# Kernel tuning notes

Hardware: AMD Instinct MI355X
Metric: run time of the kernel (lower is better)

## Reference

```python
import jax, jax.numpy as jnp
import numpy as np

D_MODEL = 768
D_COND = 128
N_LAYERS = 6
D_STATE = 16
D_CONV = 4
EXPAND = 2
D_INNER = EXPAND * D_MODEL            # 1536
DT_RANK = (D_MODEL + 15) // 16        # 48
BATCH, SEQ = 2, 1024
EPS = 1e-5


def setup_inputs() -> dict:
    key = jax.random.key(0)
    ks = iter(jax.random.split(key, 24))
    rn = lambda shape, s=0.02: jax.random.normal(next(ks), shape, dtype=jnp.float32) * s
    inp = {}
    inp["x"] = jax.random.normal(next(ks), (BATCH, SEQ, D_MODEL), dtype=jnp.float32)
    inp["condition"] = jax.random.normal(next(ks), (BATCH, D_COND), dtype=jnp.float32)
    # per-layer Mamba params, stacked on leading layer dim
    inp["in_proj_w"] = rn((N_LAYERS, 2 * D_INNER, D_MODEL))
    inp["conv_w"] = rn((N_LAYERS, D_INNER, D_CONV), 0.1)
    inp["conv_b"] = jnp.zeros((N_LAYERS, D_INNER), jnp.float32)
    inp["x_proj_w"] = rn((N_LAYERS, DT_RANK + 2 * D_STATE, D_INNER))
    inp["dt_proj_w"] = rn((N_LAYERS, D_INNER, DT_RANK), 0.1)
    inp["dt_proj_b"] = jnp.full((N_LAYERS, D_INNER), -4.0, jnp.float32)  # softplus -> small dt
    inp["A_log"] = jnp.tile(jnp.log(jnp.arange(1, D_STATE + 1, dtype=jnp.float32))[None, None, :], (N_LAYERS, D_INNER, 1))
    inp["D_skip"] = jnp.ones((N_LAYERS, D_INNER), jnp.float32)
    inp["out_proj_w"] = rn((N_LAYERS, D_MODEL, D_INNER))
    # post-residual LayerNorm affine per layer
    inp["norm_w"] = jnp.ones((N_LAYERS, D_MODEL), jnp.float32)
    inp["norm_b"] = jnp.zeros((N_LAYERS, D_MODEL), jnp.float32)
    # AdaLN: condition -> (scale, shift)
    inp["adaln_w"] = rn((N_LAYERS, 2 * D_MODEL, D_COND))
    inp["adaln_b"] = jnp.zeros((N_LAYERS, 2 * D_MODEL), jnp.float32)
    inp["final_norm_w"] = jnp.ones((D_MODEL,), jnp.float32)
    inp["final_norm_b"] = jnp.zeros((D_MODEL,), jnp.float32)
    return inp


def _ln(h, w, b):
    mu = jnp.mean(h, -1, keepdims=True)
    var = jnp.mean(jnp.square(h - mu), -1, keepdims=True)
    return (h - mu) * jax.lax.rsqrt(var + EPS) * w + b


def _ln_noaffine(h):
    mu = jnp.mean(h, -1, keepdims=True)
    var = jnp.mean(jnp.square(h - mu), -1, keepdims=True)
    return (h - mu) * jax.lax.rsqrt(var + EPS)


def _mamba(x, in_w, cw, cb, xp_w, dtp_w, dtp_b, A_log, D_skip, out_w):
    b, l, _ = x.shape
    xz = jnp.einsum('bld,ed->ble', x, in_w)                 # [b,l,2*di]
    xc, z = jnp.split(xz, 2, axis=-1)
    # causal depthwise conv over time
    xc_t = jnp.transpose(xc, (0, 2, 1))                     # [b,di,l]
    xc_t = jax.lax.conv_general_dilated(
        xc_t, cw[:, None, :], window_strides=(1,), padding=[(D_CONV - 1, 0)],
        dimension_numbers=('NCH', 'OIH', 'NCH'), feature_group_count=D_INNER)
    xc = jnp.transpose(xc_t + cb[None, :, None], (0, 2, 1))  # [b,l,di]
    xc = jax.nn.silu(xc)
    dbc = jnp.einsum('bld,ed->ble', xc, xp_w)                # [b,l,dt_rank+2*ds]
    dt = dbc[..., :DT_RANK]
    Bm = dbc[..., DT_RANK:DT_RANK + D_STATE]                 # [b,l,ds]
    Cm = dbc[..., DT_RANK + D_STATE:]                        # [b,l,ds]
    dt = jax.nn.softplus(jnp.einsum('blr,dr->bld', dt, dtp_w) + dtp_b)  # [b,l,di]
    A = -jnp.exp(A_log)                                      # [di,ds]

    def step(h, ts):
        dt_t, B_t, C_t, x_t = ts                             # [b,di],[b,ds],[b,ds],[b,di]
        dA = jnp.exp(dt_t[:, :, None] * A)                   # [b,di,ds]
        h = dA * h + (dt_t * x_t)[:, :, None] * B_t[:, None, :]
        y = jnp.sum(h * C_t[:, None, :], axis=-1)            # [b,di]
        return h, y

    h0 = jnp.zeros((b, D_INNER, D_STATE), x.dtype)
    ts = (jnp.transpose(dt, (1, 0, 2)), jnp.transpose(Bm, (1, 0, 2)),
          jnp.transpose(Cm, (1, 0, 2)), jnp.transpose(xc, (1, 0, 2)))
    h_final, y = jax.lax.scan(step, h0, ts)
    y = jnp.transpose(y, (1, 0, 2)) + D_skip * xc            # [b,l,di]
    y = y * jax.nn.silu(z)
    out = jnp.einsum('bld,ed->ble', y, out_w)                # [b,l,dm]
    return out, h_final


def reference(x, condition, in_proj_w, conv_w, conv_b, x_proj_w, dt_proj_w, dt_proj_b,
              A_log, D_skip, out_proj_w, norm_w, norm_b, adaln_w, adaln_b,
              final_norm_w, final_norm_b):
    h = x
    states = []
    for i in range(N_LAYERS):
        residual = h
        m, st = _mamba(h, in_proj_w[i], conv_w[i], conv_b[i], x_proj_w[i],
                       dt_proj_w[i], dt_proj_b[i], A_log[i], D_skip[i], out_proj_w[i])
        h = _ln(residual + m, norm_w[i], norm_b[i])
        ss = condition @ adaln_w[i].T + adaln_b[i]            # [b,2*dm]
        scale, shift = jnp.split(ss, 2, axis=-1)
        h = _ln_noaffine(h) * (1.0 + scale[:, None, :]) + shift[:, None, :]
        states.append(st)
    h = _ln(h, final_norm_w, final_norm_b)
    return h, jnp.stack(states)
```

## Files before the change

### kernel.cpp

```cpp
#include <hip/hip_runtime.h>
#include <hip/hip_bf16.h>

#define NL 6
#define DM 768
#define DI 1536
#define DS 16
#define NRANK 48
#define DBC 80
#define BATCH 2
#define SEQ 1024
#define NTOK (BATCH*SEQ)
#define NCHUNK 64
#define CHLEN 16
#define XKS 8
#define XKC (DI/XKS)

typedef __attribute__((ext_vector_type(8))) short short8;
typedef __attribute__((ext_vector_type(8))) unsigned short ushort8v;
typedef __attribute__((ext_vector_type(4))) float f32x4;
typedef __attribute__((ext_vector_type(4))) unsigned short ushort4v;

__device__ inline unsigned short f2bf(float f) {
  union { float f; unsigned u; } x; x.f = f;
  unsigned r = x.u + 0x7FFF + ((x.u >> 16) & 1);
  return (unsigned short)(r >> 16);
}
__device__ inline float bf2f(unsigned short s) {
  union { unsigned u; float f; } x; x.u = ((unsigned)s) << 16;
  return x.f;
}

__device__ inline void gl_lds16(const unsigned short* g, unsigned short* l) {
  __builtin_amdgcn_global_load_lds(
      (const __attribute__((address_space(1))) unsigned int*)(g),
      (__attribute__((address_space(3))) unsigned int*)(l),
      16, 0, 0);
}

#define V_X   (NTOK * DM / 8)
#define V_INW (NL * 2 * DI * DM / 8)
#define V_OUW (NL * DM * DI / 8)
#define V_XPW (NL * DBC * DI / 8)
#define V_DTW (NL * DI * 64 / 8)
#define V_NA  (NL * DI * DS / 8)
#define V_DTA (NTOK * 64 / 8)
#define V_ALL (V_X + V_INW + V_OUW + V_XPW + V_DTW + V_NA + V_DTA)

__device__ inline ushort8v cvt8v(f32x4 a, f32x4 b) {
  union { ushort8v u8; __hip_bfloat162 h[4]; } u;
  float2 p;
  p.x = a[0]; p.y = a[1]; u.h[0] = __float22bfloat162_rn(p);
  p.x = a[2]; p.y = a[3]; u.h[1] = __float22bfloat162_rn(p);
  p.x = b[0]; p.y = b[1]; u.h[2] = __float22bfloat162_rn(p);
  p.x = b[2]; p.y = b[3]; u.h[3] = __float22bfloat162_rn(p);
  return u.u8;
}
__device__ inline void cvt8_store(const float* s, unsigned short* d, int i) {
  f32x4 a = ((const f32x4*)s)[i * 2];
  f32x4 b = ((const f32x4*)s)[i * 2 + 1];
  ((ushort8v*)d)[i] = cvt8v(a, b);
}

__global__ __launch_bounds__(256) void cvt_k(
    const float* __restrict__ x, const float* __restrict__ inw,
    const float* __restrict__ ouw, const float* __restrict__ xpw,
    const float* __restrict__ dtpw, const float* __restrict__ alog,
    unsigned short* __restrict__ xb, unsigned short* __restrict__ inwb,
    unsigned short* __restrict__ ouwb, unsigned short* __restrict__ xpwb,
    unsigned short* __restrict__ dtwb, float* __restrict__ na,
    unsigned short* __restrict__ dtA) {
  for (int i = blockIdx.x * 256 + threadIdx.x; i < V_ALL; i += gridDim.x * 256) {
    int k = i;
    if (k < V_X) { cvt8_store(x, xb, k); continue; }
    k -= V_X;
    if (k < V_INW) { cvt8_store(inw, inwb, k); continue; }
    k -= V_INW;
    if (k < V_OUW) { cvt8_store(ouw, ouwb, k); continue; }
    k -= V_OUW;
    if (k < V_XPW) { cvt8_store(xpw, xpwb, k); continue; }
    k -= V_XPW;
    if (k < V_DTW) {
      int col8 = (k & 7) * 8;
      int row = k >> 3;
      ushort8v u8;
      if (col8 < NRANK) {
        const float* src = dtpw + (size_t)row * NRANK + col8;
        f32x4 a = *(const f32x4*)src;
        f32x4 b = *(const f32x4*)(src + 4);
        u8 = cvt8v(a, b);
      } else {
        u8 = (ushort8v){0,0,0,0,0,0,0,0};
      }
      *(ushort8v*)&dtwb[(size_t)row * 64 + col8] = u8;
      continue;
    }
    k -= V_DTW;
    if (k < V_NA) {
      f32x4 a = ((const f32x4*)alog)[k * 2];
      f32x4 b = ((const f32x4*)alog)[k * 2 + 1];
      f32x4 ra, rb;
#pragma unroll
      for (int e = 0; e < 4; e++) { ra[e] = -__expf(a[e]); rb[e] = -__expf(b[e]); }
      ((f32x4*)na)[k * 2] = ra;
      ((f32x4*)na)[k * 2 + 1] = rb;
      continue;
    }
    k -= V_NA;
    ((ushort8v*)dtA)[k] = (ushort8v){0,0,0,0,0,0,0,0};
  }
}

__global__ __launch_bounds__(256) void ada_k(const float* __restrict__ cond,
                                             const float* __restrict__ aw,
                                             const float* __restrict__ ab,
                                             float* __restrict__ ss) {
  int idx = blockIdx.x * 256 + threadIdx.x;
  int e = idx % (2 * DM);
  int b = (idx / (2 * DM)) % BATCH;
  int l = idx / (BATCH * 2 * DM);
  const float* c = cond + b * 128;
  const float* wp = aw + ((size_t)l * (2 * DM) + e) * 128;
  float s = ab[l * (2 * DM) + e];
  for (int k = 0; k < 128; k++) s = fmaf(c[k], wp[k], s);
  ss[idx] = s;
}

__global__ __launch_bounds__(256) void bt128b_k(
    const unsigned short* __restrict__ A, int lda,
    const unsigned short* __restrict__ W, int ldw,
    unsigned short* __restrict__ C, int ldc,
    int K) {
  __shared__ __align__(16) unsigned short As[3][128 * 32];
  __shared__ __align__(16) unsigned short Ws[3][128 * 32];
  const int tid = threadIdx.x;
  const int bm = blockIdx.y * 128;
  const int bn = blockIdx.x * 128;
  const int lane = tid & 63;
  const int wv = tid >> 6;
  const int wm = (wv >> 1) * 64;
  const int wn = (wv & 1) * 64;
  const int fr = lane & 15;
  const int fs = lane >> 4;

  const int r0 = tid >> 2;
  const int s0 = (tid & 3) ^ (r0 & 3);

  const unsigned short* gA0 = A + (size_t)(bm + r0) * lda + s0 * 8;
  const unsigned short* gA1 = A + (size_t)(bm + r0 + 64) * lda + s0 * 8;
  const unsigned short* gW0 = W + (size_t)(bn + r0) * ldw + s0 * 8;
  const unsigned short* gW1 = W + (size_t)(bn + r0 + 64) * ldw + s0 * 8;

  f32x4 acc[4][4];
#pragma unroll
  for (int i = 0; i < 4; i++)
#pragma unroll
    for (int j = 0; j < 4; j++) acc[i][j] = (f32x4){0.f, 0.f, 0.f, 0.f};

  const int nk = K >> 5;
  gl_lds16(gA0, &As[0][0] + tid * 8);
  gl_lds16(gA1, &As[0][2048] + tid * 8);
  gl_lds16(gW0, &Ws[0][0] + tid * 8);
  gl_lds16(gW1, &Ws[0][2048] + tid * 8);
  if (nk > 1) {
    gl_lds16(gA0 + 32, &As[1][0] + tid * 8);
    gl_lds16(gA1 + 32, &As[1][2048] + tid * 8);
    gl_lds16(gW0 + 32, &Ws[1][0] + tid * 8);
    gl_lds16(gW1 + 32, &Ws[1][2048] + tid * 8);
  }

  for (int kk = 0; kk < nk; kk++) {
    const int b = kk % 3;
    if (kk + 2 < nk) {
      const int k0 = (kk + 2) * 32;
      const int nb = (kk + 2) % 3;
      gl_lds16(gA0 + k0, &As[nb][0] + tid * 8);
      gl_lds16(gA1 + k0, &As[nb][2048] + tid * 8);
      gl_lds16(gW0 + k0, &Ws[nb][0] + tid * 8);
      gl_lds16(gW1 + k0, &Ws[nb][2048] + tid * 8);
    }
    const int ahead = (nk - 1 - kk >= 2) ? 2 : (nk - 1 - kk);
    if (ahead == 2)      asm volatile("s_waitcnt vmcnt(8)" : : : "memory");
    else if (ahead == 1) asm volatile("s_waitcnt vmcnt(4)" : : : "memory");
    else                 asm volatile("s_waitcnt vmcnt(0)" : : : "memory");
    __builtin_amdgcn_s_barrier();
    __builtin_amdgcn_sched_barrier(0);

    short8 af[4], bf[4];
#pragma unroll
    for (int i = 0; i < 4; i++) {
      int rowa = wm + i * 16 + fr;
      af[i] = *(const short8*)&As[b][rowa * 32 + ((fs ^ (rowa & 3)) * 8)];
      int rowb = wn + i * 16 + fr;
      bf[i] = *(const short8*)&Ws[b][rowb * 32 + ((fs ^ (rowb & 3)) * 8)];
    }
#pragma unroll
    for (int i = 0; i < 4; i++)
#pragma unroll
      for (int j = 0; j < 4; j++)
        acc[i][j] = __builtin_amdgcn_mfma_f32_16x16x32_bf16(af[i], bf[j], acc[i][j], 0, 0, 0);

    __builtin_amdgcn_s_barrier();
  }

#pragma unroll
  for (int i = 0; i < 4; i++) {
#pragma unroll
    for (int j = 0; j < 4; j++) {
#pragma unroll
      for (int r = 0; r < 4; r++) {
        int row = bm + wm + i * 16 + fs * 4 + r;
        int col = bn + wn + j * 16 + fr;
        C[(size_t)row * ldc + col] = f2bf(acc[i][j][r]);
      }
    }
  }
}

template<int EPI>
__global__ __launch_bounds__(256) void bt64_k(
    const unsigned short* __restrict__ A, int lda,
    const unsigned short* __restrict__ W, int ldw,
    void* __restrict__ Cv, int ldc,
    int K,
    const float* __restrict__ bias,
    const float* __restrict__ resid) {
  __shared__ __align__(16) unsigned short As[3][64 * 32];
  __shared__ __align__(16) unsigned short Ws[3][64 * 32];
  const int tid = threadIdx.x;
  const int bm = blockIdx.y * 64;
  const int bn = blockIdx.x * 64;
  const int lane = tid & 63;
  const int wv = tid >> 6;
  const int wm = (wv >> 1) * 32;
  const int wn = (wv & 1) * 32;
  const int fr = lane & 15;
  const int fs = lane >> 4;

  const int r0 = tid >> 2;
  const int s0 = (tid & 3) ^ (r0 & 3);

  const unsigned short* gA = A + (size_t)(bm + r0) * lda + s0 * 8;
  const unsigned short* gW = W + (size_t)(bn + r0) * ldw + s0 * 8;

  f32x4 acc[2][2];
#pragma unroll
  for (int i = 0; i < 2; i++)
#pragma unroll
    for (int j = 0; j < 2; j++) acc[i][j] = (f32x4){0.f, 0.f, 0.f, 0.f};

  const int nk = K >> 5;
  gl_lds16(gA, &As[0][0] + tid * 8);
  gl_lds16(gW, &Ws[0][0] + tid * 8);
  if (nk > 1) {
    gl_lds16(gA + 32, &As[1][0] + tid * 8);
    gl_lds16(gW + 32, &Ws[1][0] + tid * 8);
  }

  for (int kk = 0; kk < nk; kk++) {
    const int b = kk % 3;
    if (kk + 2 < nk) {
      const int k0 = (kk + 2) * 32;
      const int nb = (kk + 2) % 3;
      gl_lds16(gA + k0, &As[nb][0] + tid * 8);
      gl_lds16(gW + k0, &Ws[nb][0] + tid * 8);
    }
    const int ahead = (nk - 1 - kk >= 2) ? 2 : (nk - 1 - kk);
    if (ahead == 2)      asm volatile("s_waitcnt vmcnt(4)" : : : "memory");
    else if (ahead == 1) asm volatile("s_waitcnt vmcnt(2)" : : : "memory");
    else                 asm volatile("s_waitcnt vmcnt(0)" : : : "memory");
    __builtin_amdgcn_s_barrier();
    __builtin_amdgcn_sched_barrier(0);

    short8 af[2], bf[2];
#pragma unroll
    for (int i = 0; i < 2; i++) {
      int rowa = wm + i * 16 + fr;
      af[i] = *(const short8*)&As[b][rowa * 32 + ((fs ^ (rowa & 3)) * 8)];
      int rowb = wn + i * 16 + fr;
      bf[i] = *(const short8*)&Ws[b][rowb * 32 + ((fs ^ (rowb & 3)) * 8)];
    }
#pragma unroll
    for (int i = 0; i < 2; i++)
#pragma unroll
      for (int j = 0; j < 2; j++)
        acc[i][j] = __builtin_amdgcn_mfma_f32_16x16x32_bf16(af[i], bf[j], acc[i][j], 0, 0, 0);

    __builtin_amdgcn_s_barrier();
  }

#pragma unroll
  for (int i = 0; i < 2; i++) {
#pragma unroll
    for (int j = 0; j < 2; j++) {
#pragma unroll
      for (int r = 0; r < 4; r++) {
        int row = bm + wm + i * 16 + fs * 4 + r;
        int col = bn + wn + j * 16 + fr;
        float v = acc[i][j][r];
        if (EPI == 1) {
          float xv = v + bias[col];
          float sp = (xv > 20.f) ? xv : log1pf(__expf(xv));
          ((unsigned short*)Cv)[(size_t)row * ldc + col] = f2bf(sp);
        }
        if (EPI == 2) {
          ((float*)Cv)[(size_t)row * ldc + col] = v + resid[(size_t)row * ldc + col];
        }
      }
    }
  }
}

__global__ __launch_bounds__(256) void xp_k(
    const unsigned short* __restrict__ A,
    const unsigned short* __restrict__ W,
    unsigned short* __restrict__ part) {
  __shared__ __align__(16) unsigned short As[64][40];
  __shared__ __align__(16) unsigned short Ws[80][40];
  const int tid = threadIdx.x;
  const int ks = blockIdx.x;
  const int bm = blockIdx.y * 64;
  const int lane = tid & 63;
  const int wv = tid >> 6;
  const int fr = lane & 15;
  const int fs = lane >> 4;
  const int fk = fs * 8;

  const int ar = tid >> 2;
  const int ac = (tid & 3) * 8;
  const int k0base = ks * XKC;

  const unsigned short* gA  = A + (size_t)(bm + ar) * DI + k0base + ac;
  const unsigned short* gW0 = W + (size_t)ar * DI + k0base + ac;
  const unsigned short* gW1 = W + (size_t)(64 + ar) * DI + k0base + ac;

  f32x4 acc[5];
#pragma unroll
  for (int n = 0; n < 5; n++) acc[n] = (f32x4){0.f, 0.f, 0.f, 0.f};

  short8 aA, w0A, w1A;
  aA = *(const short8*)(gA);
  w0A = *(const short8*)(gW0);
  if (tid < 64) w1A = *(const short8*)(gW1);

  const int nk = XKC / 32;
  for (int kk = 0; kk < nk; kk++) {
    __syncthreads();
    *(short8*)&As[ar][ac] = aA;
    *(short8*)&Ws[ar][ac] = w0A;
    if (tid < 64) *(short8*)&Ws[64 + ar][ac] = w1A;
    __syncthreads();

    if (kk + 1 < nk) {
      const int k0 = (kk + 1) * 32;
      aA = *(const short8*)(gA + k0);
      w0A = *(const short8*)(gW0 + k0);
      if (tid < 64) w1A = *(const short8*)(gW1 + k0);
    }

    short8 af = *(const short8*)&As[wv * 16 + fr][fk];
#pragma unroll
    for (int n = 0; n < 5; n++) {
      short8 bf = *(const short8*)&Ws[n * 16 + fr][fk];
      acc[n] = __builtin_amdgcn_mfma_f32_16x16x32_bf16(af, bf, acc[n], 0, 0, 0);
    }
  }

#pragma unroll
  for (int n = 0; n < 5; n++) {
#pragma unroll
    for (int r = 0; r < 4; r++) {
      int row = bm + wv * 16 + fs * 4 + r;
      part[((size_t)ks * NTOK + row) * DBC + n * 16 + fr] = f2bf(acc[n][r]);
    }
  }
}

__global__ __launch_bounds__(256) void xp_reduce_k(const unsigned short* __restrict__ part,
                                                   unsigned short* __restrict__ dtA,
                                                   unsigned short* __restrict__ bc) {
  int i = blockIdx.x * 256 + threadIdx.x;
  const ushort4v* p4 = (const ushort4v*)part;
  const int stride4 = NTOK * DBC / 4;
  float s0 = 0.f, s1 = 0.f, s2 = 0.f, s3 = 0.f;
#pragma unroll
  for (int ks = 0; ks < XKS; ks++) {
    ushort4v v = p4[(size_t)ks * stride4 + i];
    s0 += bf2f(v[0]); s1 += bf2f(v[1]); s2 += bf2f(v[2]); s3 += bf2f(v[3]);
  }
  ushort4v o;
  o[0] = f2bf(s0); o[1] = f2bf(s1); o[2] = f2bf(s2); o[3] = f2bf(s3);
  int c4 = (i * 4) % DBC;
  int m = (i * 4) / DBC;
  if (c4 < NRANK) {
    *(ushort4v*)&dtA[(size_t)m * 64 + c4] = o;
  } else {
    *(ushort4v*)&bc[(size_t)m * 32 + (c4 - NRANK)] = o;
  }
}

__global__ __launch_bounds__(256) void conv_silu_k(const unsigned short* __restrict__ xz,
                                                   const float* __restrict__ cw,
                                                   const float* __restrict__ cb,
                                                   unsigned short* __restrict__ xcb) {
  const int d0 = (blockIdx.x * 256 + threadIdx.x) * 2;
  const int l0 = blockIdx.y * 16;
  const int b = blockIdx.z;
  const size_t mbase = (size_t)b * SEQ;
  const float wa0 = cw[d0 * 4 + 0], wa1 = cw[d0 * 4 + 1];
  const float wa2 = cw[d0 * 4 + 2], wa3 = cw[d0 * 4 + 3];
  const float wb0 = cw[d0 * 4 + 4], wb1 = cw[d0 * 4 + 5];
  const float wb2 = cw[d0 * 4 + 6], wb3 = cw[d0 * 4 + 7];
  const float ba = cb[d0], bb = cb[d0 + 1];

  float a3 = 0.f, a2 = 0.f, a1 = 0.f, b3 = 0.f, b2 = 0.f, b1 = 0.f;
  if (l0 >= 3) { ushort2 u = *(const ushort2*)&xz[(mbase + l0 - 3) * (2 * DI) + d0]; a3 = bf2f(u.x); b3 = bf2f(u.y); }
  if (l0 >= 2) { ushort2 u = *(const ushort2*)&xz[(mbase + l0 - 2) * (2 * DI) + d0]; a2 = bf2f(u.x); b2 = bf2f(u.y); }
  if (l0 >= 1) { ushort2 u = *(const ushort2*)&xz[(mbase + l0 - 1) * (2 * DI) + d0]; a1 = bf2f(u.x); b1 = bf2f(u.y); }
#pragma unroll
  for (int t = 0; t < 16; t++) {
    const int l = l0 + t;
    ushort2 u = *(const ushort2*)&xz[(mbase + l) * (2 * DI) + d0];
    float ca = bf2f(u.x), cbv = bf2f(u.y);
    float sa = ba + wa0 * a3 + wa1 * a2 + wa2 * a1 + wa3 * ca;
    float sb = bb + wb0 * b3 + wb1 * b2 + wb2 * b1 + wb3 * cbv;
    float ra = sa / (1.f + __expf(-sa));
    float rb = sb / (1.f + __expf(-sb));
    ushort2 o; o.x = f2bf(ra); o.y = f2bf(rb);
    *(ushort2*)&xcb[(mbase + l) * DI + d0] = o;
    a3 = a2; a2 = a1; a1 = ca;
    b3 = b2; b2 = b1; b1 = cbv;
  }
}

__global__ __launch_bounds__(256) void scan1_k(const unsigned short* __restrict__ dt,
                                               const unsigned short* __restrict__ xc,
                                               const unsigned short* __restrict__ bc,
                                               const float* __restrict__ negA_l,
                                               unsigned int* __restrict__ ch_pk,
                                               unsigned int* __restrict__ yc_pk) {
  __shared__ float Bs[CHLEN][DS];
  __shared__ float Cs[CHLEN][DS];
  const int tid = threadIdx.x;
  const int j = blockIdx.x;
  const int cg = blockIdx.y;
  const int b = cg / 6;
  const int d = (cg % 6) * 256 + tid;
  const int c = b * DI + d;
  const int m0 = b * SEQ + j * CHLEN;

  for (int e = tid; e < CHLEN * 32; e += 256) {
    int row = e >> 5, col = e & 31;
    float v = bf2f(bc[(size_t)(m0 + row) * 32 + col]);
    if (col < DS) Bs[row][col] = v; else Cs[row][col - DS] = v;
  }

  float Av[DS];
  const float* na = negA_l + (size_t)d * DS;
#pragma unroll
  for (int s = 0; s < DS; s++) Av[s] = na[s];
  const float Av0 = Av[0];
  bool fast = true;
#pragma unroll
  for (int s = 0; s < DS; s++)
    fast = fast && (fabsf(Av[s] - (s + 1) * Av0) <= 1e-4f * (s + 1));

  float dts[CHLEN], xcs[CHLEN];
#pragma unroll
  for (int t = 0; t < CHLEN; t++) {
    dts[t] = bf2f(dt[(size_t)(m0 + t) * DI + d]);
    xcs[t] = bf2f(xc[(size_t)(m0 + t) * DI + d]);
  }
  __syncthreads();

  float h[DS];
#pragma unroll
  for (int s = 0; s < DS; s++) h[s] = 0.f;
  float cd = 0.f;

  for (int t = 0; t < CHLEN; t++) {
    float dtv = dts[t];
    cd += dtv;
    float dtx = dtv * xcs[t];
    float ysum = 0.f;
    if (fast) {
      float e1 = __expf(dtv * Av0);
      float dA = e1;
      h[0] = fmaf(dA, h[0], dtx * Bs[t][0]);
      ysum = fmaf(h[0], Cs[t][0], ysum);
#pragma unroll
      for (int s = 1; s < DS; s++) {
        dA *= e1;
        h[s] = fmaf(dA, h[s], dtx * Bs[t][s]);
        ysum = fmaf(h[s], Cs[t][s], ysum);
      }
    } else {
#pragma unroll
      for (int s = 0; s < DS; s++) {
        float dA = __expf(dtv * Av[s]);
        h[s] = fmaf(dA, h[s], dtx * Bs[t][s]);
        ysum = fmaf(h[s], Cs[t][s], ysum);
      }
    }
    yc_pk[(size_t)(m0 + t) * DI + d] =
        (unsigned int)f2bf(ysum) | ((unsigned int)f2bf(cd) << 16);
  }

  size_t base = ((size_t)j * (BATCH * DI) + c) * DS;
#pragma unroll
  for (int s = 0; s < DS; s++) {
    unsigned int pk = (unsigned int)f2bf(__expf(cd * Av[s]))
                    | ((unsigned int)f2bf(h[s]) << 16);
    ch_pk[base + s] = pk;
  }
}

__global__ __launch_bounds__(256) void scan2_k(const unsigned int* __restrict__ ch_pk,
                                               unsigned short* __restrict__ hin,
                                               float* __restrict__ states_out) {
  int idx = blockIdx.x * 256 + threadIdx.x;
  const int stride = BATCH * DI * DS;
  float h = 0.f;
  for (int j = 0; j < NCHUNK; j++) {
    hin[(size_t)j * stride + idx] = f2bf(h);
    unsigned int pk = ch_pk[(size_t)j * stride + idx];
    float ca = bf2f((unsigned short)(pk & 0xFFFF));
    float hl = bf2f((unsigned short)(pk >> 16));
    h = fmaf(ca, h, hl);
  }
  states_out[idx] = h;
}

__global__ __launch_bounds__(256) void scanfix_k(const unsigned int* __restrict__ yc_pk,
                                                 const unsigned short* __restrict__ xc,
                                                 const unsigned short* __restrict__ xz,
                                                 const unsigned short* __restrict__ bc,
                                                 const float* __restrict__ negA_l,
                                                 const float* __restrict__ Dsk,
                                                 const unsigned short* __restrict__ hin,
                                                 unsigned short* __restrict__ y) {
  int idx = blockIdx.x * 256 + threadIdx.x;
  int d = idx % DI;
  int m = idx / DI;
  int b = m / SEQ;
  int j = (m % SEQ) / CHLEN;
  unsigned int pk = yc_pk[idx];
  float yv = bf2f((unsigned short)(pk & 0xFFFF));
  float cd = bf2f((unsigned short)(pk >> 16));
  const f32x4* na4 = (const f32x4*)(negA_l + (size_t)d * DS);
  const ushort4v* cp4 = (const ushort4v*)(bc + (size_t)m * 32 + DS);
  const ushort4v* h4 = (const ushort4v*)(hin + ((size_t)j * (BATCH * DI) + (size_t)b * DI + d) * DS);
  float corr = 0.f;
#pragma unroll
  for (int q = 0; q < 4; q++) {
    f32x4 na = na4[q];
    ushort4v cp = cp4[q];
    ushort4v hh = h4[q];
#pragma unroll
    for (int e = 0; e < 4; e++)
      corr = fmaf(__expf(cd * na[e]) * bf2f(hh[e]), bf2f(cp[e]), corr);
  }
  yv += corr;
  float xv = bf2f(xc[idx]);
  float zv = bf2f(xz[(size_t)m * (2 * DI) + DI + d]);
  float sig = 1.f / (1.f + __expf(-zv));
  y[idx] = f2bf((yv + Dsk[d] * xv) * (zv * sig));
}

template<bool ADA>
__global__ __launch_bounds__(256) void ln_k(const float* __restrict__ in,
                                            const float* __restrict__ w,
                                            const float* __restrict__ bb,
                                            const float* __restrict__ ss,
                                            float* __restrict__ out,
                                            unsigned short* __restrict__ outb) {
  __shared__ float red[8];
  const int row = blockIdx.x;
  const int bt = row / SEQ;
  const int tid = threadIdx.x;
  const float* x = in + (size_t)row * DM;
  float v[3];
#pragma unroll
  for (int i = 0; i < 3; i++) v[i] = x[tid + i * 256];
  float s1 = v[0] + v[1] + v[2];
  float s2 = v[0]*v[0] + v[1]*v[1] + v[2]*v[2];
#pragma unroll
  for (int o = 32; o > 0; o >>= 1) { s1 += __shfl_down(s1, o); s2 += __shfl_down(s2, o); }
  int wv = tid >> 6, ln = tid & 63;
  if (ln == 0) { red[wv*2] = s1; red[wv*2+1] = s2; }
  __syncthreads();
  s1 = red[0] + red[2] + red[4] + red[6];
  s2 = red[1] + red[3] + red[5] + red[7];
  float mu = s1 * (1.f / DM);
  float var = s2 * (1.f / DM) - mu * mu;
  float rs = rsqrtf(var + 1e-5f);
  float t[3];
#pragma unroll
  for (int i = 0; i < 3; i++) {
    int c = tid + i * 256;
    t[i] = (v[i] - mu) * rs * w[c] + bb[c];
  }
  if (!ADA) {
#pragma unroll
    for (int i = 0; i < 3; i++) out[(size_t)row * DM + tid + i * 256] = t[i];
    return;
  }
  __syncthreads();
  s1 = t[0] + t[1] + t[2];
  s2 = t[0]*t[0] + t[1]*t[1] + t[2]*t[2];
#pragma unroll
  for (int o = 32; o > 0; o >>= 1) { s1 += __shfl_down(s1, o); s2 += __shfl_down(s2, o); }
  if (ln == 0) { red[wv*2] = s1; red[wv*2+1] = s2; }
  __syncthreads();
  s1 = red[0] + red[2] + red[4] + red[6];
  s2 = red[1] + red[3] + red[5] + red[7];
  float mu2 = s1 * (1.f / DM);
  float var2 = s2 * (1.f / DM) - mu2 * mu2;
  float rs2 = rsqrtf(var2 + 1e-5f);
#pragma unroll
  for (int i = 0; i < 3; i++) {
    int c = tid + i * 256;
    float sc = ss[bt * (2 * DM) + c];
    float sh = ss[bt * (2 * DM) + DM + c];
    float r = (t[i] - mu2) * rs2 * (1.f + sc) + sh;
    out[(size_t)row * DM + c] = r;
    outb[(size_t)row * DM + c] = f2bf(r);
  }
}

extern "C" void kernel_launch(void* const* d_in, const int* in_sizes, int n_in,
                              void* d_out, int out_size, void* d_ws, size_t ws_size,
                              hipStream_t stream) {
  const float* x      = (const float*)d_in[0];
  const float* cond   = (const float*)d_in[1];
  const float* in_w   = (const float*)d_in[2];
  const float* conv_w = (const float*)d_in[3];
  const float* conv_b = (const float*)d_in[4];
  const float* xp_w   = (const float*)d_in[5];
  const float* dtp_w  = (const float*)d_in[6];
  const float* dtp_b  = (const float*)d_in[7];
  const float* A_log  = (const float*)d_in[8];
  const float* Dsk    = (const float*)d_in[9];
  const float* out_w  = (const float*)d_in[10];
  const float* norm_w = (const float*)d_in[11];
  const float* norm_b = (const float*)d_in[12];
  const float* ada_w  = (const float*)d_in[13];
  const float* ada_b  = (const float*)d_in[14];
  const float* fn_w   = (const float*)d_in[15];
  const float* fn_b   = (const float*)d_in[16];

  float* out_h = (float*)d_out;
  float* out_states = out_h + (size_t)NTOK * DM;

  float* p = (float*)d_ws;
  float* h_cur = p; p += (size_t)NTOK * DM;
  float* res2  = p; p += (size_t)NTOK * DM;
  float* ss    = p; p += (size_t)NL * BATCH * 2 * DM;
  float* negA  = p; p += (size_t)NL * DI * DS;
  unsigned int* ch_pk = (unsigned int*)p; p += (size_t)NCHUNK * BATCH * DI * DS;
  unsigned int* yc_pk = (unsigned int*)p; p += (size_t)NTOK * DI;
  unsigned short* q = (unsigned short*)p;
  unsigned short* hin      = q; q += (size_t)NCHUNK * BATCH * DI * DS;
  unsigned short* in_w_bf  = q; q += (size_t)NL * 2 * DI * DM;
  unsigned short* out_w_bf = q; q += (size_t)NL * DM * DI;
  unsigned short* xp_w_bf  = q; q += (size_t)NL * DBC * DI;
  unsigned short* dtw_bf   = q; q += (size_t)NL * DI * 64;
  unsigned short* h_bf     = q; q += (size_t)NTOK * DM;
  unsigned short* xz_bf    = q; q += (size_t)NTOK * 2 * DI;
  unsigned short* xc_bf    = q; q += (size_t)NTOK * DI;
  unsigned short* dtb_bf   = q; q += (size_t)NTOK * DI;
  unsigned short* yb_bf    = q; q += (size_t)NTOK * DI;
  unsigned short* part_bf  = q; q += (size_t)XKS * NTOK * DBC;
  unsigned short* dtA_bf   = q; q += (size_t)NTOK * 64;
  unsigned short* bc_bf    = q; q += (size_t)NTOK * 32;

  cvt_k<<<2048, 256, 0, stream>>>(x, in_w, out_w, xp_w, dtp_w, A_log,
                                  h_bf, in_w_bf, out_w_bf, xp_w_bf, dtw_bf,
                                  negA, dtA_bf);
  ada_k<<<72, 256, 0, stream>>>(cond, ada_w, ada_b, ss);

  for (int l = 0; l < NL; l++) {
    bt128b_k<<<dim3(24, 16), 256, 0, stream>>>(
        h_bf, DM, in_w_bf + (size_t)l * 2 * DI * DM, DM, xz_bf, 2 * DI, DM);
    conv_silu_k<<<dim3(DI / 512, SEQ / 16, BATCH), 256, 0, stream>>>(
        xz_bf, conv_w + (size_t)l * DI * 4, conv_b + (size_t)l * DI, xc_bf);
    xp_k<<<dim3(XKS, NTOK / 64), 256, 0, stream>>>(
        xc_bf, xp_w_bf + (size_t)l * DBC * DI, part_bf);
    xp_reduce_k<<<NTOK * DBC / 4 / 256, 256, 0, stream>>>(part_bf, dtA_bf, bc_bf);
    bt64_k<1><<<dim3(DI / 64, NTOK / 64), 256, 0, stream>>>(
        dtA_bf, 64, dtw_bf + (size_t)l * DI * 64, 64, dtb_bf, DI,
        64, dtp_b + (size_t)l * DI, nullptr);
    scan1_k<<<dim3(NCHUNK, 12), 256, 0, stream>>>(
        dtb_bf, xc_bf, bc_bf, negA + (size_t)l * DI * DS, ch_pk, yc_pk);
    scan2_k<<<192, 256, 0, stream>>>(
        ch_pk, hin, out_states + (size_t)l * BATCH * DI * DS);
    scanfix_k<<<NTOK * DI / 256, 256, 0, stream>>>(
        yc_pk, xc_bf, xz_bf, bc_bf, negA + (size_t)l * DI * DS,
        Dsk + (size_t)l * DI, hin, yb_bf);
    bt64_k<2><<<dim3(DM / 64, NTOK / 64), 256, 0, stream>>>(
        yb_bf, DI, out_w_bf + (size_t)l * DM * DI, DI, res2, DM,
        DI, nullptr, (l == 0) ? x : h_cur);
    ln_k<true><<<NTOK, 256, 0, stream>>>(
        res2, norm_w + (size_t)l * DM, norm_b + (size_t)l * DM,
        ss + (size_t)l * BATCH * 2 * DM, h_cur, h_bf);
  }
  ln_k<false><<<NTOK, 256, 0, stream>>>(h_cur, fn_w, fn_b, nullptr, out_h, nullptr);
}
```

Before: 747.2 us.

## Split-K out_proj GEMM, fold AdaLN into conversion kernel, batch scan2 loads

The out_proj GEMM now splits K into two halves across blockIdx.z and writes two fp32 partials. The following LayerNorm kernel sums both partials plus the residual, so the grid doubles from 384 blocks and fills more CUs. The AdaLN projection kernel is merged into the initial conversion kernel to save one launch. scan2 prefetches eight chunk states at a time to hide load latency. The cost is an extra fp32 partial buffer round-trip per layer.

```diff
diff --git a/kernel.cpp b/kernel.cpp
--- a/kernel.cpp
+++ b/kernel.cpp
@@ -44,7 +44,8 @@
 #define V_DTW (NL * DI * 64 / 8)
 #define V_NA  (NL * DI * DS / 8)
 #define V_DTA (NTOK * 64 / 8)
-#define V_ALL (V_X + V_INW + V_OUW + V_XPW + V_DTW + V_NA + V_DTA)
+#define V_ADA (NL * BATCH * 2 * DM)
+#define V_ALL (V_X + V_INW + V_OUW + V_XPW + V_DTW + V_NA + V_DTA + V_ADA)
 
 __device__ inline ushort8v cvt8v(f32x4 a, f32x4 b) {
   union { ushort8v u8; __hip_bfloat162 h[4]; } u;
@@ -65,10 +66,12 @@
     const float* __restrict__ x, const float* __restrict__ inw,
     const float* __restrict__ ouw, const float* __restrict__ xpw,
     const float* __restrict__ dtpw, const float* __restrict__ alog,
+    const float* __restrict__ cond, const float* __restrict__ adaw,
+    const float* __restrict__ adab,
     unsigned short* __restrict__ xb, unsigned short* __restrict__ inwb,
     unsigned short* __restrict__ ouwb, unsigned short* __restrict__ xpwb,
     unsigned short* __restrict__ dtwb, float* __restrict__ na,
-    unsigned short* __restrict__ dtA) {
+    unsigned short* __restrict__ dtA, float* __restrict__ ss) {
   for (int i = blockIdx.x * 256 + threadIdx.x; i < V_ALL; i += gridDim.x * 256) {
     int k = i;
     if (k < V_X) { cvt8_store(x, xb, k); continue; }
@@ -106,23 +109,22 @@
       continue;
     }
     k -= V_NA;
-    ((ushort8v*)dtA)[k] = (ushort8v){0,0,0,0,0,0,0,0};
-  }
-}
-
-__global__ __launch_bounds__(256) void ada_k(const float* __restrict__ cond,
-                                             const float* __restrict__ aw,
-                                             const float* __restrict__ ab,
-                                             float* __restrict__ ss) {
-  int idx = blockIdx.x * 256 + threadIdx.x;
-  int e = idx % (2 * DM);
-  int b = (idx / (2 * DM)) % BATCH;
-  int l = idx / (BATCH * 2 * DM);
-  const float* c = cond + b * 128;
-  const float* wp = aw + ((size_t)l * (2 * DM) + e) * 128;
-  float s = ab[l * (2 * DM) + e];
-  for (int k = 0; k < 128; k++) s = fmaf(c[k], wp[k], s);
-  ss[idx] = s;
+    if (k < V_DTA) {
+      ((ushort8v*)dtA)[k] = (ushort8v){0,0,0,0,0,0,0,0};
+      continue;
+    }
+    k -= V_DTA;
+    {
+      int e = k % (2 * DM);
+      int b = (k / (2 * DM)) % BATCH;
+      int l = k / (BATCH * 2 * DM);
+      const float* c = cond + b * 128;
+      const float* wp = adaw + ((size_t)l * (2 * DM) + e) * 128;
+      float s = adab[l * (2 * DM) + e];
+      for (int kk = 0; kk < 128; kk++) s = fmaf(c[kk], wp[kk], s);
+      ss[k] = s;
+    }
+  }
 }
 
 __global__ __launch_bounds__(256) void bt128b_k(
@@ -222,13 +224,13 @@
     const unsigned short* __restrict__ W, int ldw,
     void* __restrict__ Cv, int ldc,
     int K,
-    const float* __restrict__ bias,
-    const float* __restrict__ resid) {
+    const float* __restrict__ bias) {
   __shared__ __align__(16) unsigned short As[3][64 * 32];
   __shared__ __align__(16) unsigned short Ws[3][64 * 32];
   const int tid = threadIdx.x;
   const int bm = blockIdx.y * 64;
   const int bn = blockIdx.x * 64;
+  const int kz = (EPI == 3) ? blockIdx.z : 0;
   const int lane = tid & 63;
   const int wv = tid >> 6;
   const int wm = (wv >> 1) * 32;
@@ -239,8 +241,8 @@
   const int r0 = tid >> 2;
   const int s0 = (tid & 3) ^ (r0 & 3);
 
-  const unsigned short* gA = A + (size_t)(bm + r0) * lda + s0 * 8;
-  const unsigned short* gW = W + (size_t)(bn + r0) * ldw + s0 * 8;
+  const unsigned short* gA = A + (size_t)(bm + r0) * lda + kz * K + s0 * 8;
+  const unsigned short* gW = W + (size_t)(bn + r0) * ldw + kz * K + s0 * 8;
 
   f32x4 acc[2][2];
 #pragma unroll
@@ -302,8 +304,8 @@
           float sp = (xv > 20.f) ? xv : log1pf(__expf(xv));
           ((unsigned short*)Cv)[(size_t)row * ldc + col] = f2bf(sp);
         }
-        if (EPI == 2) {
-          ((float*)Cv)[(size_t)row * ldc + col] = v + resid[(size_t)row * ldc + col];
+        if (EPI == 3) {
+          ((float*)Cv)[((size_t)kz * NTOK + row) * ldc + col] = v;
         }
       }
     }
@@ -520,12 +522,17 @@
   int idx = blockIdx.x * 256 + threadIdx.x;
   const int stride = BATCH * DI * DS;
   float h = 0.f;
-  for (int j = 0; j < NCHUNK; j++) {
-    hin[(size_t)j * stride + idx] = f2bf(h);
-    unsigned int pk = ch_pk[(size_t)j * stride + idx];
-    float ca = bf2f((unsigned short)(pk & 0xFFFF));
-    float hl = bf2f((unsigned short)(pk >> 16));
-    h = fmaf(ca, h, hl);
+  for (int g = 0; g < NCHUNK / 8; g++) {
+    unsigned int pks[8];
+#pragma unroll
+    for (int u = 0; u < 8; u++)
+      pks[u] = ch_pk[(size_t)(g * 8 + u) * stride + idx];
+#pragma unroll
+    for (int u = 0; u < 8; u++) {
+      hin[(size_t)(g * 8 + u) * stride + idx] = f2bf(h);
+      h = fmaf(bf2f((unsigned short)(pks[u] & 0xFFFF)), h,
+               bf2f((unsigned short)(pks[u] >> 16)));
+    }
   }
   states_out[idx] = h;
 }
@@ -568,6 +575,7 @@
 
 template<bool ADA>
 __global__ __launch_bounds__(256) void ln_k(const float* __restrict__ in,
+                                            const float* __restrict__ resid,
                                             const float* __restrict__ w,
                                             const float* __restrict__ bb,
                                             const float* __restrict__ ss,
@@ -577,10 +585,17 @@
   const int row = blockIdx.x;
   const int bt = row / SEQ;
   const int tid = threadIdx.x;
-  const float* x = in + (size_t)row * DM;
   float v[3];
 #pragma unroll
-  for (int i = 0; i < 3; i++) v[i] = x[tid + i * 256];
+  for (int i = 0; i < 3; i++) {
+    int c = tid + i * 256;
+    if (ADA) {
+      v[i] = in[(size_t)row * DM + c] + in[(size_t)(NTOK + row) * DM + c]
+           + resid[(size_t)row * DM + c];
+    } else {
+      v[i] = in[(size_t)row * DM + c];
+    }
+  }
   float s1 = v[0] + v[1] + v[2];
   float s2 = v[0]*v[0] + v[1]*v[1] + v[2]*v[2];
 #pragma unroll
@@ -653,7 +668,7 @@
 
   float* p = (float*)d_ws;
   float* h_cur = p; p += (size_t)NTOK * DM;
-  float* res2  = p; p += (size_t)NTOK * DM;
+  float* part2 = p; p += (size_t)2 * NTOK * DM;
   float* ss    = p; p += (size_t)NL * BATCH * 2 * DM;
   float* negA  = p; p += (size_t)NL * DI * DS;
   unsigned int* ch_pk = (unsigned int*)p; p += (size_t)NCHUNK * BATCH * DI * DS;
@@ -674,9 +689,9 @@
   unsigned short* bc_bf    = q; q += (size_t)NTOK * 32;
 
   cvt_k<<<2048, 256, 0, stream>>>(x, in_w, out_w, xp_w, dtp_w, A_log,
+                                  cond, ada_w, ada_b,
                                   h_bf, in_w_bf, out_w_bf, xp_w_bf, dtw_bf,
-                                  negA, dtA_bf);
-  ada_k<<<72, 256, 0, stream>>>(cond, ada_w, ada_b, ss);
+                                  negA, dtA_bf, ss);
 
   for (int l = 0; l < NL; l++) {
     bt128b_k<<<dim3(24, 16), 256, 0, stream>>>(
@@ -688,7 +703,7 @@
     xp_reduce_k<<<NTOK * DBC / 4 / 256, 256, 0, stream>>>(part_bf, dtA_bf, bc_bf);
     bt64_k<1><<<dim3(DI / 64, NTOK / 64), 256, 0, stream>>>(
         dtA_bf, 64, dtw_bf + (size_t)l * DI * 64, 64, dtb_bf, DI,
-        64, dtp_b + (size_t)l * DI, nullptr);
+        64, dtp_b + (size_t)l * DI);
     scan1_k<<<dim3(NCHUNK, 12), 256, 0, stream>>>(
         dtb_bf, xc_bf, bc_bf, negA + (size_t)l * DI * DS, ch_pk, yc_pk);
     scan2_k<<<192, 256, 0, stream>>>(
@@ -696,12 +711,14 @@
     scanfix_k<<<NTOK * DI / 256, 256, 0, stream>>>(
         yc_pk, xc_bf, xz_bf, bc_bf, negA + (size_t)l * DI * DS,
         Dsk + (size_t)l * DI, hin, yb_bf);
-    bt64_k<2><<<dim3(DM / 64, NTOK / 64), 256, 0, stream>>>(
-        yb_bf, DI, out_w_bf + (size_t)l * DM * DI, DI, res2, DM,
-        DI, nullptr, (l == 0) ? x : h_cur);
+    bt64_k<3><<<dim3(DM / 64, NTOK / 64, 2), 256, 0, stream>>>(
+        yb_bf, DI, out_w_bf + (size_t)l * DM * DI, DI, part2, DM,
+        DI / 2, nullptr);
     ln_k<true><<<NTOK, 256, 0, stream>>>(
-        res2, norm_w + (size_t)l * DM, norm_b + (size_t)l * DM,
+        part2, (l == 0) ? x : h_cur,
+        norm_w + (size_t)l * DM, norm_b + (size_t)l * DM,
         ss + (size_t)l * BATCH * 2 * DM, h_cur, h_bf);
   }
-  ln_k<false><<<NTOK, 256, 0, stream>>>(h_cur, fn_w, fn_b, nullptr, out_h, nullptr);
-}
+  ln_k<false><<<NTOK, 256, 0, stream>>>(h_cur, nullptr, fn_w, fn_b, nullptr,
+                                        out_h, nullptr);
+}
```

New measurement: 696.9 us. 1.07x faster.
